# Performance work log

Hardware: AMD Instinct MI355X
Metric: run time of the kernel (lower is better)

Reference implementation:

```python
import jax, jax.numpy as jnp
import numpy as np
from jax import lax

B, C, H, W = 8, 384, 64, 64


def cos_map(N):
    # ortho DCT-II basis: weight[n, x] = cos(n*(x+0.5)*pi/N) * sqrt(2/N), row 0 /= sqrt(2)
    wx = (jnp.arange(N, dtype=jnp.float32) + 0.5) / N
    wn = jnp.arange(N, dtype=jnp.float32)[:, None]
    w = jnp.cos(wn * wx[None, :] * jnp.pi) * np.sqrt(2.0 / N).astype(np.float32)
    return w.at[0, :].multiply(np.float32(1.0 / np.sqrt(2.0)))


def setup_inputs() -> dict:
    key = jax.random.key(0)
    ks = jax.random.split(key, 8)
    s = 0.05
    return {
        "x": jax.random.normal(ks[0], (B, C, H, W), jnp.float32),
        "freq_embed": jax.random.normal(ks[1], (H, W, C), jnp.float32),
        "dw_w": jax.random.normal(ks[2], (C, 1, 3, 3), jnp.float32) * s,
        "dw_b": jnp.zeros((C,), jnp.float32),
        "lin_w": jax.random.normal(ks[3], (2 * C, C), jnp.float32) * s,
        "lin_b": jnp.zeros((2 * C,), jnp.float32),
        "tok_w": jax.random.normal(ks[4], (C, C), jnp.float32) * s,
        "tok_b": jnp.zeros((C,), jnp.float32),
        "c": jnp.ones((1,), jnp.float32),
        "alpha": jnp.ones((1,), jnp.float32) * 0.1,
        "ln_g": jnp.ones((C,), jnp.float32),
        "ln_b": jnp.zeros((C,), jnp.float32),
        "out_w": jax.random.normal(ks[5], (C, C), jnp.float32) * s,
        "out_b": jnp.zeros((C,), jnp.float32),
    }


def reference(x, freq_embed, dw_w, dw_b, lin_w, lin_b, tok_w, tok_b, c, alpha, ln_g, ln_b, out_w, out_b):
    Bc, Cc, Hc, Wc = x.shape
    # depthwise 3x3 conv
    x = lax.conv_general_dilated(x, dw_w, (1, 1), 'SAME',
                                 feature_group_count=Cc,
                                 dimension_numbers=('NCHW', 'OIHW', 'NCHW'))
    x = x + dw_b[None, :, None, None]
    # linear to 2C (channels-last), split into signal x and gate z
    xz = jnp.einsum('bchw,dc->bhwd', x, lin_w) + lin_b
    xs, z = xz[..., :Cc], xz[..., Cc:]          # [B,H,W,C]
    xs = jnp.transpose(xs, (0, 3, 1, 2))        # [B,C,H,W]
    # 2D ortho DCT-II: D = Wh @ x @ Ww^T
    Wh, Ww = cos_map(Hc), cos_map(Wc)
    Xd = jnp.einsum('nh,bchw,kw->bcnk', Wh, xs, Ww)
    # learned frequency gating: t = ReLU(Linear(freq_embed)), per (H,W,C)
    t = jax.nn.relu(jnp.einsum('hwc,dc->hwd', freq_embed, tok_w) + tok_b)
    ct = jnp.transpose(jnp.cos(c * t), (2, 0, 1))[None]        # [1,C,H,W]
    st = jnp.transpose(jnp.sin(c * t), (2, 0, 1))[None] / c[0]
    # x_u0 == x_v0 == Xd in the original (dct2d applied twice to same x)
    final = ct * Xd + st * (Xd + 0.5 * alpha[0] * Xd)
    # 2D inverse DCT: x = Wh^T @ D @ Ww
    xi = jnp.einsum('nh,bcnk,kw->bchw', Wh, final, Ww)
    # LayerNorm over channels, gate with SiLU(z), output linear
    y = jnp.transpose(xi, (0, 2, 3, 1))          # [B,H,W,C]
    mu = jnp.mean(y, axis=-1, keepdims=True)
    var = jnp.mean((y - mu) ** 2, axis=-1, keepdims=True)
    y = (y - mu) * lax.rsqrt(var + 1e-5) * ln_g + ln_b
    y = y * jax.nn.silu(z)
    y = jnp.einsum('bhwc,dc->bhwd', y, out_w) + out_b
    return jnp.transpose(y, (0, 3, 1, 2))        # [B,C,H,W]
```

## Files before the change

kernel.cpp:

```cpp
#include <hip/hip_runtime.h>

typedef _Float16 h2 __attribute__((ext_vector_type(2)));
typedef _Float16 h4 __attribute__((ext_vector_type(4)));
typedef _Float16 h8 __attribute__((ext_vector_type(8)));
typedef float    f4 __attribute__((ext_vector_type(4)));

#define MFMA32(a,b,c) __builtin_amdgcn_mfma_f32_16x16x32_f16((a),(b),(c),0,0,0)
#define MFMA16(a,b,c) __builtin_amdgcn_mfma_f32_16x16x16f16((a),(b),(c),0,0,0)

#define B_N 8
#define C_N 384
#define P_N 4096
#define PI_F 3.14159265358979323846f

__device__ __forceinline__ h4 to_h4(f4 v) {
  h4 r; r[0]=(_Float16)v[0]; r[1]=(_Float16)v[1]; r[2]=(_Float16)v[2]; r[3]=(_Float16)v[3];
  return r;
}

__device__ __forceinline__ void gl_lds16(const _Float16* g, _Float16* l) {
  __builtin_amdgcn_global_load_lds(
      (const __attribute__((address_space(1))) void*)g,
      (__attribute__((address_space(3))) void*)l, 16, 0, 0);
}

__device__ __forceinline__ void gemm_step(
    const _Float16* __restrict__ ga, const _Float16* __restrict__ gb,
    int kc, bool pref,
    _Float16* laC, _Float16* lbC, _Float16* laN, _Float16* lbN,
    int wave, int s_row, int wm, int wn, int l15, int quad, f4 (&acc)[4][4]) {
  if (pref) {
    #pragma unroll
    for (int s = 0; s < 2; s++) {
      int seg = wave * 2 + s;
      int row = seg * 16 + s_row;
      int lane = (threadIdx.x & 63);
      gl_lds16(ga + (size_t)row*384 + kc + 32, &laN[seg*512 + lane*8]);
      gl_lds16(gb + (size_t)row*384 + kc + 32, &lbN[seg*512 + lane*8]);
    }
  }
  h8 af[4], bf[4];
  #pragma unroll
  for (int i = 0; i < 4; i++) {
    af[i] = *(const h8*)&laC[(wm*64 + i*16 + l15)*32 + quad*8];
    bf[i] = *(const h8*)&lbC[(wn*64 + i*16 + l15)*32 + quad*8];
  }
  #pragma unroll
  for (int i = 0; i < 4; i++)
  #pragma unroll
  for (int j = 0; j < 4; j++)
    acc[i][j] = MFMA32(af[i], bf[j], acc[i][j]);
  __syncthreads();
}

__global__ __launch_bounds__(256) void k_setup(
    const float* __restrict__ lin_w, const float* __restrict__ tok_w,
    const float* __restrict__ out_w, _Float16* __restrict__ lwh,
    _Float16* __restrict__ twh, _Float16* __restrict__ owh,
    _Float16* __restrict__ wmg, _Float16* __restrict__ wmtg) {
  int t = blockIdx.x * 256 + threadIdx.x;
  if (t < 768*384) lwh[t] = (_Float16)lin_w[t];
  if (t < 384*384) { twh[t] = (_Float16)tok_w[t]; owh[t] = (_Float16)out_w[t]; }
  if (t < 4096) {
    int n = t >> 6, h = t & 63;
    float v = cosf((float)n * ((float)h + 0.5f) * (PI_F / 64.0f)) * 0.1767766952966369f;
    if (n == 0) v *= 0.7071067811865476f;
    wmg[n*64 + h]  = (_Float16)v;
    wmtg[h*64 + n] = (_Float16)v;
  }
}

__global__ __launch_bounds__(256) void k_dwconv(
    const float* __restrict__ x, const float* __restrict__ dww,
    const float* __restrict__ dwb, _Float16* __restrict__ xdw) {
  int blk = blockIdx.x;
  int h = blk & 63;
  int rest = blk >> 6;
  int cgi = rest % 6;
  int b = rest / 6;
  int c0 = cgi * 64;
  int t = threadIdx.x;
  int w = t & 63, ci = t >> 6;
  __shared__ _Float16 buf[64 * 68];
  const float* xb = x + (size_t)b * C_N * P_N;
  int wl = (w > 0)  ? w - 1 : 0;
  int wr = (w < 63) ? w + 1 : 63;
  #pragma unroll
  for (int j = 0; j < 8; j++) {
    int lc = ci * 16 + j * 2;
    h2 pr;
    #pragma unroll
    for (int e = 0; e < 2; e++) {
      int c = c0 + lc + e;
      const float* xc = xb + (size_t)c * P_N;
      float k0=dww[c*9+0],k1=dww[c*9+1],k2=dww[c*9+2];
      float k3=dww[c*9+3],k4=dww[c*9+4],k5=dww[c*9+5];
      float k6=dww[c*9+6],k7=dww[c*9+7],k8=dww[c*9+8];
      float top = (h > 0)  ? xc[(h-1)*64 + w] : 0.0f;
      float mid = xc[h*64 + w];
      float bot = (h < 63) ? xc[(h+1)*64 + w] : 0.0f;
      float tl = __shfl(top, wl, 64), tr = __shfl(top, wr, 64);
      float ml = __shfl(mid, wl, 64), mr = __shfl(mid, wr, 64);
      float bl = __shfl(bot, wl, 64), br = __shfl(bot, wr, 64);
      if (w == 0)  { tl = 0.f; ml = 0.f; bl = 0.f; }
      if (w == 63) { tr = 0.f; mr = 0.f; br = 0.f; }
      float acc = dwb[c];
      acc += k0*tl + k1*top + k2*tr;
      acc += k3*ml + k4*mid + k5*mr;
      acc += k6*bl + k7*bot + k8*br;
      pr[e] = (_Float16)acc;
    }
    *(h2*)&buf[w*68 + lc] = pr;
  }
  __syncthreads();
  _Float16* op = xdw + ((size_t)b*P_N + h*64) * C_N + c0;
  #pragma unroll
  for (int i = 0; i < 4; i++) {
    int flat = (t + 256*i) * 4;
    int pix = flat >> 6, cl = flat & 63;
    *(h4*)&op[(size_t)pix*C_N + cl] = *(const h4*)&buf[pix*68 + cl];
  }
}

__global__ __launch_bounds__(256) void k_gate(
    const float* __restrict__ fe, const _Float16* __restrict__ twh,
    const float* __restrict__ tkb, const float* __restrict__ cc,
    const float* __restrict__ aa, _Float16* __restrict__ g) {
  int pt = blockIdx.x & 63, dt = blockIdx.x >> 6;
  int p0 = pt*64, d0 = dt*64;
  int t = threadIdx.x, lane = t & 63, wave = t >> 6;
  int quad = lane >> 4, l15 = lane & 15;
  int wm_ = wave >> 1, wn = wave & 1;
  __shared__ _Float16 la[64*40], lb[64*40];
  int srow = t >> 2, scg = (t & 3) * 8;
  f4 acc[2][2] = {};
  for (int kc = 0; kc < 384; kc += 32) {
    const float* src = fe + (size_t)(p0 + srow)*384 + kc + scg;
    f4 v0 = *(const f4*)src;
    f4 v1 = *(const f4*)(src + 4);
    h8 hv;
    hv[0]=(_Float16)v0[0]; hv[1]=(_Float16)v0[1]; hv[2]=(_Float16)v0[2]; hv[3]=(_Float16)v0[3];
    hv[4]=(_Float16)v1[0]; hv[5]=(_Float16)v1[1]; hv[6]=(_Float16)v1[2]; hv[7]=(_Float16)v1[3];
    *(h8*)&la[srow*40 + scg] = hv;
    *(h8*)&lb[srow*40 + scg] = *(const h8*)&twh[(size_t)(d0 + srow)*384 + kc + scg];
    __syncthreads();
    h8 a0 = *(const h8*)&la[(wm_*32 + l15)*40 + quad*8];
    h8 a1 = *(const h8*)&la[(wm_*32 + 16 + l15)*40 + quad*8];
    h8 b0 = *(const h8*)&lb[(wn*32 + l15)*40 + quad*8];
    h8 b1 = *(const h8*)&lb[(wn*32 + 16 + l15)*40 + quad*8];
    acc[0][0] = MFMA32(a0, b0, acc[0][0]);
    acc[0][1] = MFMA32(a0, b1, acc[0][1]);
    acc[1][0] = MFMA32(a1, b0, acc[1][0]);
    acc[1][1] = MFMA32(a1, b1, acc[1][1]);
    __syncthreads();
  }
  float c0 = cc[0];
  float s1 = (1.0f + 0.5f*aa[0]) / c0;
  #pragma unroll
  for (int i = 0; i < 2; i++)
  #pragma unroll
  for (int j = 0; j < 2; j++) {
    int d  = d0 + wn*32 + j*16 + l15;
    int pl = wm_*32 + i*16 + quad*4;
    float bias = tkb[d];
    h4 hv;
    #pragma unroll
    for (int r = 0; r < 4; r++) {
      float tv = fmaxf(acc[i][j][r] + bias, 0.0f);
      hv[r] = (_Float16)(__cosf(c0*tv) + s1*__sinf(c0*tv));
    }
    *(h4*)&g[(size_t)d*P_N + p0 + pl] = hv;
  }
}

__global__ __launch_bounds__(256) void k_gemm1(
    const _Float16* __restrict__ xdw, const _Float16* __restrict__ lwh,
    const float* __restrict__ lnb, _Float16* __restrict__ xs,
    _Float16* __restrict__ zs) {
  int pt = blockIdx.x & 31;
  int rest = blockIdx.x >> 5;
  int dt = rest % 6, b = rest / 6;
  int p0 = pt * 128, d0 = dt * 128;
  int t = threadIdx.x, lane = t & 63, wave = t >> 6;
  int quad = lane >> 4, l15 = lane & 15;
  int wm = wave >> 1, wn = wave & 1;
  __shared__ _Float16 la0[128 * 32], lb0[128 * 32];
  __shared__ _Float16 la1[128 * 32], lb1[128 * 32];
  int s_row = lane >> 2;
  int s_col = (lane & 3) * 8;
  const _Float16* ga = xdw + ((size_t)b*P_N + p0) * 384 + s_col;
  const _Float16* gb = lwh + (size_t)d0 * 384 + s_col;
  f4 acc[4][4] = {};
  #pragma unroll
  for (int s = 0; s < 2; s++) {
    int seg = wave * 2 + s;
    int row = seg * 16 + s_row;
    gl_lds16(ga + (size_t)row*384, &la0[seg*512 + lane*8]);
    gl_lds16(gb + (size_t)row*384, &lb0[seg*512 + lane*8]);
  }
  __syncthreads();
  #pragma unroll
  for (int kt = 0; kt < 6; kt++) {
    int kc = kt * 64;
    gemm_step(ga, gb, kc,      true,            la0, lb0, la1, lb1,
              wave, s_row, wm, wn, l15, quad, acc);
    gemm_step(ga, gb, kc + 32, (kc + 64 < 384), la1, lb1, la0, lb0,
              wave, s_row, wm, wn, l15, quad, acc);
  }
  bool isz = (d0 >= 384);
  #pragma unroll
  for (int j = 0; j < 4; j++) {
    int d = d0 + wn*64 + j*16 + l15;
    float bias = lnb[d];
    _Float16* dst = isz ? (zs + ((size_t)b*C_N + (d-384)) * P_N)
                        : (xs + ((size_t)b*C_N + d) * P_N);
    #pragma unroll
    for (int i = 0; i < 4; i++) {
      int p = p0 + wm*64 + i*16 + quad*4;
      h4 hv;
      if (isz) {
        #pragma unroll
        for (int r = 0; r < 4; r++) {
          float v = acc[i][j][r] + bias;
          v = v / (1.0f + __expf(-v));
          hv[r] = (_Float16)v;
        }
      } else {
        #pragma unroll
        for (int r = 0; r < 4; r++) hv[r] = (_Float16)(acc[i][j][r] + bias);
      }
      *(h4*)&dst[p] = hv;
    }
  }
}

__global__ __launch_bounds__(256) void k_dct(
    const _Float16* __restrict__ xs, const _Float16* __restrict__ g,
    const _Float16* __restrict__ wmg, const _Float16* __restrict__ wmtg,
    _Float16* __restrict__ xi) {
  int b = blockIdx.x / 96, cg = blockIdx.x % 96;
  int c0 = cg * 4;
  int t = threadIdx.x, wave = t >> 6, lane = t & 63;
  int quad = lane >> 4, l15 = lane & 15;
  __shared__ _Float16 wm_s[64*72];
  __shared__ _Float16 wmt_s[64*72];
  __shared__ _Float16 pb[4][64*72];
  for (int i = t; i < 512; i += 256) {
    int row = i >> 3, col = (i & 7) * 8;
    *(h8*)&wm_s[row*72 + col]  = *(const h8*)&wmg[row*64 + col];
    *(h8*)&wmt_s[row*72 + col] = *(const h8*)&wmtg[row*64 + col];
  }
  const _Float16* xsb = xs + ((size_t)b*C_N + c0) * P_N;
  for (int i = t; i < 2048; i += 256) {
    int pl = i >> 9, idx = i & 511;
    int p = idx * 8, hh = p >> 6, ww = p & 63;
    *(h8*)&pb[pl][hh*72 + ww] = *(const h8*)&xsb[(size_t)pl*P_N + p];
  }
  __syncthreads();
  h8 aS[4][2], bW[4][2];
  #pragma unroll
  for (int I = 0; I < 4; I++)
  #pragma unroll
  for (int kk = 0; kk < 2; kk++) {
    aS[I][kk] = *(const h8*)&pb[wave][(I*16 + l15)*72 + kk*32 + quad*8];
    bW[I][kk] = *(const h8*)&wm_s[(I*16 + l15)*72 + kk*32 + quad*8];
  }
  h4 t1h[4][4];
  #pragma unroll
  for (int I = 0; I < 4; I++)
  #pragma unroll
  for (int J = 0; J < 4; J++) {
    f4 a = {};
    a = MFMA32(aS[I][0], bW[J][0], a);
    a = MFMA32(aS[I][1], bW[J][1], a);
    t1h[I][J] = to_h4(a);
  }
  __syncthreads();
  const _Float16* gb = g + (size_t)c0 * P_N;
  for (int i = t; i < 2048; i += 256) {
    int pl = i >> 9, idx = i & 511;
    int p = idx * 8, hh = p >> 6, ww = p & 63;
    *(h8*)&pb[pl][hh*72 + ww] = *(const h8*)&gb[(size_t)pl*P_N + p];
  }
  __syncthreads();
  f4 t2[4][4] = {};
  #pragma unroll
  for (int I = 0; I < 4; I++)
  #pragma unroll
  for (int K4 = 0; K4 < 4; K4++) {
    h4 af = *(const h4*)&wm_s[(I*16 + l15)*72 + K4*16 + quad*4];
    #pragma unroll
    for (int J = 0; J < 4; J++) t2[I][J] = MFMA16(af, t1h[K4][J], t2[I][J]);
  }
  h4 fh[4][4];
  #pragma unroll
  for (int I = 0; I < 4; I++)
  #pragma unroll
  for (int J = 0; J < 4; J++) {
    int n0 = I*16 + quad*4, k = J*16 + l15;
    h4 r;
    #pragma unroll
    for (int rr = 0; rr < 4; rr++) {
      float gv = (float)pb[wave][(n0+rr)*72 + k];
      r[rr] = (_Float16)(t2[I][J][rr] * gv);
    }
    fh[I][J] = r;
  }
  f4 t3[4][4] = {};
  #pragma unroll
  for (int J = 0; J < 4; J++)
  #pragma unroll
  for (int K4 = 0; K4 < 4; K4++) {
    h4 bf = *(const h4*)&wmt_s[(J*16 + l15)*72 + K4*16 + quad*4];
    #pragma unroll
    for (int I = 0; I < 4; I++) t3[I][J] = MFMA16(fh[K4][I], bf, t3[I][J]);
  }
  h4 t3h[4][4];
  #pragma unroll
  for (int I = 0; I < 4; I++)
  #pragma unroll
  for (int J = 0; J < 4; J++) t3h[I][J] = to_h4(t3[I][J]);
  f4 t4[4][4] = {};
  #pragma unroll
  for (int I = 0; I < 4; I++)
  #pragma unroll
  for (int K4 = 0; K4 < 4; K4++) {
    h4 af = *(const h4*)&wmt_s[(I*16 + l15)*72 + K4*16 + quad*4];
    #pragma unroll
    for (int J = 0; J < 4; J++) t4[I][J] = MFMA16(af, t3h[K4][J], t4[I][J]);
  }
  #pragma unroll
  for (int I = 0; I < 4; I++)
  #pragma unroll
  for (int J = 0; J < 4; J++) {
    int w0 = I*16 + quad*4, hq = J*16 + l15;
    *(h4*)&pb[wave][hq*72 + w0] = to_h4(t4[I][J]);
  }
  __syncthreads();
  _Float16* xib = xi + ((size_t)b*C_N + c0) * P_N;
  for (int i = t; i < 2048; i += 256) {
    int pl = i >> 9, idx = i & 511;
    int p = idx * 8, hh = p >> 6, ww = p & 63;
    *(h8*)&xib[(size_t)pl*P_N + p] = *(const h8*)&pb[pl][hh*72 + ww];
  }
}

__global__ __launch_bounds__(256) void k_ubuild(
    const _Float16* __restrict__ xi, const _Float16* __restrict__ zs,
    const float* __restrict__ lng, const float* __restrict__ lnbv,
    _Float16* __restrict__ u) {
  int b = blockIdx.x >> 6, pt = blockIdx.x & 63;
  int p0 = pt * 64;
  int t = threadIdx.x;
  __shared__ _Float16 ut[64 * 392];
  __shared__ float red[4][64], red2[4][64];
  __shared__ float muL[64], rsL[64];
  int cr = t >> 3;
  int px0 = (t & 7) * 8;
  const _Float16* xib = xi + (size_t)b * C_N * P_N;
  #pragma unroll
  for (int i = 0; i < 12; i++) {
    int c = cr + 32 * i;
    h8 v = *(const h8*)&xib[(size_t)c * P_N + p0 + px0];
    #pragma unroll
    for (int e = 0; e < 8; e++) ut[(px0 + e) * 392 + c] = v[e];
  }
  __syncthreads();
  int px = t & 63, seg = t >> 6;
  float s = 0.f, ss = 0.f;
  #pragma unroll
  for (int j = 0; j < 12; j++) {
    h8 v = *(const h8*)&ut[px * 392 + seg * 96 + j * 8];
    #pragma unroll
    for (int e = 0; e < 8; e++) { float f = (float)v[e]; s += f; ss += f * f; }
  }
  red[seg][px] = s; red2[seg][px] = ss;
  __syncthreads();
  if (t < 64) {
    float st  = red[0][t] + red[1][t] + red[2][t] + red[3][t];
    float sst = red2[0][t] + red2[1][t] + red2[2][t] + red2[3][t];
    float m = st * (1.f/384.f);
    float var = sst * (1.f/384.f) - m * m;
    muL[t] = m; rsL[t] = rsqrtf(var + 1e-5f);
  }
  __syncthreads();
  const _Float16* zb = zs + (size_t)b * C_N * P_N;
  #pragma unroll
  for (int i = 0; i < 12; i++) {
    int c = cr + 32 * i;
    float g = lng[c], bb = lnbv[c];
    h8 zv = *(const h8*)&zb[(size_t)c * P_N + p0 + px0];
    #pragma unroll
    for (int e = 0; e < 8; e++) {
      int p = px0 + e;
      float y = ((float)ut[p * 392 + c] - muL[p]) * rsL[p] * g + bb;
      ut[p * 392 + c] = (_Float16)(y * (float)zv[e]);
    }
  }
  __syncthreads();
  _Float16* ub = u + ((size_t)b * P_N + p0) * C_N;
  #pragma unroll
  for (int i = 0; i < 12; i++) {
    int idx = t + 256 * i;
    int row = idx / 48, ch = idx % 48;
    *(h8*)&ub[(size_t)row * C_N + ch * 8] = *(const h8*)&ut[row * 392 + ch * 8];
  }
}

__global__ __launch_bounds__(256) void k_gemm2(
    const _Float16* __restrict__ u, const _Float16* __restrict__ owh,
    const float* __restrict__ ob, float* __restrict__ out) {
  int pt = blockIdx.x & 31;
  int rest = blockIdx.x >> 5;
  int dt = rest % 3, b = rest / 3;
  int p0 = pt * 128, d0 = dt * 128;
  int t = threadIdx.x, lane = t & 63, wave = t >> 6;
  int quad = lane >> 4, l15 = lane & 15;
  int wm = wave >> 1, wn = wave & 1;
  __shared__ _Float16 la0[128 * 32], lb0[128 * 32];
  __shared__ _Float16 la1[128 * 32], lb1[128 * 32];
  int s_row = lane >> 2;
  int s_col = (lane & 3) * 8;
  const _Float16* ga = u   + ((size_t)b*P_N + p0) * 384 + s_col;
  const _Float16* gb = owh + (size_t)d0 * 384 + s_col;
  f4 acc[4][4] = {};
  #pragma unroll
  for (int s = 0; s < 2; s++) {
    int seg = wave * 2 + s;
    int row = seg * 16 + s_row;
    gl_lds16(ga + (size_t)row*384, &la0[seg*512 + lane*8]);
    gl_lds16(gb + (size_t)row*384, &lb0[seg*512 + lane*8]);
  }
  __syncthreads();
  #pragma unroll
  for (int kt = 0; kt < 6; kt++) {
    int kc = kt * 64;
    gemm_step(ga, gb, kc,      true,            la0, lb0, la1, lb1,
              wave, s_row, wm, wn, l15, quad, acc);
    gemm_step(ga, gb, kc + 32, (kc + 64 < 384), la1, lb1, la0, lb0,
              wave, s_row, wm, wn, l15, quad, acc);
  }
  #pragma unroll
  for (int j = 0; j < 4; j++) {
    int d = d0 + wn*64 + j*16 + l15;
    float bias = ob[d];
    #pragma unroll
    for (int i = 0; i < 4; i++) {
      int p = p0 + wm*64 + i*16 + quad*4;
      f4 v;
      #pragma unroll
      for (int r = 0; r < 4; r++) v[r] = acc[i][j][r] + bias;
      *(f4*)&out[((size_t)b*C_N + d)*P_N + p] = v;
    }
  }
}

extern "C" void kernel_launch(void* const* d_in, const int* in_sizes, int n_in,
                              void* d_out, int out_size, void* d_ws, size_t ws_size,
                              hipStream_t stream) {
  (void)in_sizes; (void)n_in; (void)out_size; (void)ws_size;
  const float* x    = (const float*)d_in[0];
  const float* fe   = (const float*)d_in[1];
  const float* dww  = (const float*)d_in[2];
  const float* dwb  = (const float*)d_in[3];
  const float* linw = (const float*)d_in[4];
  const float* linb = (const float*)d_in[5];
  const float* tokw = (const float*)d_in[6];
  const float* tokb = (const float*)d_in[7];
  const float* cc   = (const float*)d_in[8];
  const float* aa   = (const float*)d_in[9];
  const float* lng  = (const float*)d_in[10];
  const float* lnbv = (const float*)d_in[11];
  const float* outw = (const float*)d_in[12];
  const float* outb = (const float*)d_in[13];
  float* out = (float*)d_out;

  char* ws = (char*)d_ws;
  size_t off = 0;
  auto alloc = [&](size_t bytes) -> void* {
    void* p = ws + off;
    off += (bytes + 255) & ~(size_t)255;
    return p;
  };
  _Float16* lwh  = (_Float16*)alloc((size_t)768*384*2);
  _Float16* twh  = (_Float16*)alloc((size_t)384*384*2);
  _Float16* owh  = (_Float16*)alloc((size_t)384*384*2);
  _Float16* wmg  = (_Float16*)alloc((size_t)64*64*2);
  _Float16* wmtg = (_Float16*)alloc((size_t)64*64*2);
  _Float16* xdw  = (_Float16*)alloc((size_t)B_N*P_N*C_N*2);
  _Float16* xs   = (_Float16*)alloc((size_t)B_N*C_N*P_N*2);
  _Float16* zs   = (_Float16*)alloc((size_t)B_N*C_N*P_N*2);
  _Float16* gg   = (_Float16*)alloc((size_t)C_N*P_N*2);
  _Float16* xi   = xdw;
  _Float16* uu   = xs;

  k_setup<<<1152, 256, 0, stream>>>(linw, tokw, outw, lwh, twh, owh, wmg, wmtg);
  k_dwconv<<<3072, 256, 0, stream>>>(x, dww, dwb, xdw);
  k_gate<<<384, 256, 0, stream>>>(fe, twh, tokb, cc, aa, gg);
  k_gemm1<<<1536, 256, 0, stream>>>(xdw, lwh, linb, xs, zs);
  k_dct<<<768, 256, 0, stream>>>(xs, gg, wmg, wmtg, xi);
  k_ubuild<<<512, 256, 0, stream>>>(xi, zs, lng, lnbv, uu);
  k_gemm2<<<768, 256, 0, stream>>>(uu, owh, outb, out);
}
```

Before: 258.7 us.

## Swizzle GEMM LDS tiles and overlap prefetch with fine-grained vmcnt waits

```diff
diff --git a/kernel.cpp b/kernel.cpp
--- a/kernel.cpp
+++ b/kernel.cpp
@@ -26,31 +26,42 @@
 
 __device__ __forceinline__ void gemm_step(
     const _Float16* __restrict__ ga, const _Float16* __restrict__ gb,
-    int kc, bool pref,
+    int kcn, bool pref,
     _Float16* laC, _Float16* lbC, _Float16* laN, _Float16* lbN,
-    int wave, int s_row, int wm, int wn, int l15, int quad, f4 (&acc)[4][4]) {
+    f4 (&acc)[4][4]) {
+  int t = threadIdx.x, lane = t & 63, wave = t >> 6;
+  int quad = lane >> 4, l15 = lane & 15;
+  int wm = wave >> 1, wn = wave & 1;
+  int s_row = lane >> 2;
   if (pref) {
     #pragma unroll
     for (int s = 0; s < 2; s++) {
       int seg = wave * 2 + s;
       int row = seg * 16 + s_row;
-      int lane = (threadIdx.x & 63);
-      gl_lds16(ga + (size_t)row*384 + kc + 32, &laN[seg*512 + lane*8]);
-      gl_lds16(gb + (size_t)row*384 + kc + 32, &lbN[seg*512 + lane*8]);
-    }
-  }
+      gl_lds16(ga + (size_t)row*384 + kcn, &laN[seg*512 + lane*8]);
+      gl_lds16(gb + (size_t)row*384 + kcn, &lbN[seg*512 + lane*8]);
+    }
+    asm volatile("s_waitcnt vmcnt(4)" ::: "memory");
+  } else {
+    asm volatile("s_waitcnt vmcnt(0)" ::: "memory");
+  }
+  __builtin_amdgcn_s_barrier();
+  asm volatile("" ::: "memory");
   h8 af[4], bf[4];
+  int sq = (quad ^ (l15 & 3)) * 8;
   #pragma unroll
   for (int i = 0; i < 4; i++) {
-    af[i] = *(const h8*)&laC[(wm*64 + i*16 + l15)*32 + quad*8];
-    bf[i] = *(const h8*)&lbC[(wn*64 + i*16 + l15)*32 + quad*8];
-  }
+    af[i] = *(const h8*)&laC[(wm*64 + i*16 + l15)*32 + sq];
+    bf[i] = *(const h8*)&lbC[(wn*64 + i*16 + l15)*32 + sq];
+  }
+  asm volatile("s_waitcnt lgkmcnt(0)" ::: "memory");
+  __builtin_amdgcn_s_barrier();
+  asm volatile("" ::: "memory");
   #pragma unroll
   for (int i = 0; i < 4; i++)
   #pragma unroll
   for (int j = 0; j < 4; j++)
     acc[i][j] = MFMA32(af[i], bf[j], acc[i][j]);
-  __syncthreads();
 }
 
 __global__ __launch_bounds__(256) void k_setup(
@@ -187,9 +198,9 @@
   __shared__ _Float16 la0[128 * 32], lb0[128 * 32];
   __shared__ _Float16 la1[128 * 32], lb1[128 * 32];
   int s_row = lane >> 2;
-  int s_col = (lane & 3) * 8;
-  const _Float16* ga = xdw + ((size_t)b*P_N + p0) * 384 + s_col;
-  const _Float16* gb = lwh + (size_t)d0 * 384 + s_col;
+  int scol2 = (((lane & 3) ^ (s_row & 3)) * 8);
+  const _Float16* ga = xdw + ((size_t)b*P_N + p0) * 384 + scol2;
+  const _Float16* gb = lwh + (size_t)d0 * 384 + scol2;
   f4 acc[4][4] = {};
   #pragma unroll
   for (int s = 0; s < 2; s++) {
@@ -198,14 +209,11 @@
     gl_lds16(ga + (size_t)row*384, &la0[seg*512 + lane*8]);
     gl_lds16(gb + (size_t)row*384, &lb0[seg*512 + lane*8]);
   }
-  __syncthreads();
   #pragma unroll
   for (int kt = 0; kt < 6; kt++) {
     int kc = kt * 64;
-    gemm_step(ga, gb, kc,      true,            la0, lb0, la1, lb1,
-              wave, s_row, wm, wn, l15, quad, acc);
-    gemm_step(ga, gb, kc + 32, (kc + 64 < 384), la1, lb1, la0, lb0,
-              wave, s_row, wm, wn, l15, quad, acc);
+    gemm_step(ga, gb, kc + 32,  true,            la0, lb0, la1, lb1, acc);
+    gemm_step(ga, gb, kc + 64,  (kc + 64 < 384), la1, lb1, la0, lb0, acc);
   }
   bool isz = (d0 >= 384);
   #pragma unroll
@@ -420,9 +428,9 @@
   __shared__ _Float16 la0[128 * 32], lb0[128 * 32];
   __shared__ _Float16 la1[128 * 32], lb1[128 * 32];
   int s_row = lane >> 2;
-  int s_col = (lane & 3) * 8;
-  const _Float16* ga = u   + ((size_t)b*P_N + p0) * 384 + s_col;
-  const _Float16* gb = owh + (size_t)d0 * 384 + s_col;
+  int scol2 = (((lane & 3) ^ (s_row & 3)) * 8);
+  const _Float16* ga = u   + ((size_t)b*P_N + p0) * 384 + scol2;
+  const _Float16* gb = owh + (size_t)d0 * 384 + scol2;
   f4 acc[4][4] = {};
   #pragma unroll
   for (int s = 0; s < 2; s++) {
@@ -431,14 +439,11 @@
     gl_lds16(ga + (size_t)row*384, &la0[seg*512 + lane*8]);
     gl_lds16(gb + (size_t)row*384, &lb0[seg*512 + lane*8]);
   }
-  __syncthreads();
   #pragma unroll
   for (int kt = 0; kt < 6; kt++) {
     int kc = kt * 64;
-    gemm_step(ga, gb, kc,      true,            la0, lb0, la1, lb1,
-              wave, s_row, wm, wn, l15, quad, acc);
-    gemm_step(ga, gb, kc + 32, (kc + 64 < 384), la1, lb1, la0, lb0,
-              wave, s_row, wm, wn, l15, quad, acc);
+    gemm_step(ga, gb, kc + 32,  true,            la0, lb0, la1, lb1, acc);
+    gemm_step(ga, gb, kc + 64,  (kc + 64 < 384), la1, lb1, la0, lb0, acc);
   }
   #pragma unroll
   for (int j = 0; j < 4; j++) {
```

After: 255.3 us. About the same (-1.3%).
